# Optimization experiments

Measured on AMD Instinct MI355X. Metric: run time of the kernel, lower is better.

The kernel has to match this reference:

```python
import jax, jax.numpy as jnp
import numpy as np

HEADS = 8
DIM = 64
L = 2
P = 4  # hard-coded p_num in the torch module


def conv2d(x, w, b=None, pad=0, groups=1):
    y = jax.lax.conv_general_dilated(x, w, (1, 1), [(pad, pad), (pad, pad)],
        dimension_numbers=('NCHW', 'OIHW', 'NCHW'), feature_group_count=groups)
    return y if b is None else y + b[None, :, None, None]


def conv3d(x, w, pad=1, groups=1):
    return jax.lax.conv_general_dilated(x, w, (1, 1, 1), [(pad, pad)] * 3,
        dimension_numbers=('NCDHW', 'OIDHW', 'NCDHW'), feature_group_count=groups)


def pw(x, w):  # 1x1 conv, w: [O, C]
    return jnp.einsum('oc,bchw->bohw', w, x)


def layernorm(x, w, b):  # WithBias_LayerNorm over channel dim of NCHW
    mu = x.mean(axis=1, keepdims=True)
    var = ((x - mu) ** 2).mean(axis=1, keepdims=True)
    return (x - mu) / jnp.sqrt(var + 1e-5) * w[None, :, None, None] + b[None, :, None, None]


def l2n(x):  # F.normalize(dim=-1, p=2)
    return x / jnp.maximum(jnp.linalg.norm(x, axis=-1, keepdims=True), 1e-12)


def gelu(x):
    return jax.nn.gelu(x, approximate=False)


def spec_attn(x, mask, wq, wk, wv, dwq, dwk, dwv, resc, wp, mp1, mp2):
    b, c, h, w = x.shape
    ch = c // HEADS
    q = conv2d(pw(x, wq), dwq, pad=1, groups=c).reshape(b, HEADS, ch, h * w)
    k = conv2d(pw(x, wk), dwk, pad=1, groups=c).reshape(b, HEADS, ch, h * w)
    v = conv2d(pw(x, wv), dwv, pad=1, groups=c).reshape(b, HEADS, ch, h * w)
    q, k = l2n(q), l2n(k)
    att = jnp.einsum('bhcn,bhdn->bhcd', q, k) * resc[None, :, None, None]
    mb = pw(jax.nn.relu(conv2d(mask, mp1, pad=1)), mp2).mean(axis=(2, 3)).reshape(b, HEADS, ch)
    att = att + mb[:, :, None, :] - mb[:, :, :, None]
    att = jax.nn.softmax(att, axis=-1)
    out = jnp.einsum('bhcd,bhdn->bhcn', att, v).reshape(b, c, h, w)
    return pw(out, wp)


def ffn2d(x, w1, w2):  # PreNorm: dwconv3x3 (groups=dim, out=4*dim) -> GELU -> 1x1
    return pw(gelu(conv2d(x, w1, pad=1, groups=DIM)), w2)


def pol_attn(x, mask, wq, wk, wv, pwt, pb, resc, m1w, m1b, m2w, m2b):
    bp, c, h, w = x.shape
    bn = bp // P
    ch = c // HEADS
    xt = x.reshape(bn, P, c, h, w).transpose(0, 3, 4, 1, 2).reshape(bn * h * w, P, c)
    def heads_(t):
        return t.reshape(-1, P, HEADS, ch).transpose(0, 2, 1, 3)
    q = l2n(heads_(xt @ wq.T))
    k = l2n(heads_(xt @ wk.T))
    v = heads_(xt @ wv.T)
    att = jnp.einsum('bhpc,bhqc->bhpq', q, k) * resc[None, :, None, None]
    mg = pw(gelu(conv2d(mask, m1w, m1b, pad=1, groups=c)), m2w) + m2b[None, :, None, None]
    mg = mg.reshape(bn, P, c, h, w).mean(axis=2).transpose(0, 2, 3, 1).reshape(bn * h * w, P)
    att = att + (mg[:, None, :] - mg[:, :, None])[:, None]
    att = jax.nn.softmax(att, axis=-1)
    o = jnp.einsum('bhpq,bhqc->bhpc', att, v).transpose(0, 2, 1, 3).reshape(-1, P, c)
    o = o @ pwt.T + pb
    return o.reshape(bn, h, w, P, c).transpose(0, 3, 4, 1, 2).reshape(bp, c, h, w)


def ffn3d(x, w1, w2):  # PreNorm_Pols: 3D dwconv over (p,h,w) -> GELU -> 1x1x1
    bp, c, h, w = x.shape
    bn = bp // P
    y = x.reshape(bn, P, c, h, w).transpose(0, 2, 1, 3, 4)  # [bn, c, p, h, w]
    y = gelu(conv3d(y, w1, pad=1, groups=DIM))
    y = jnp.einsum('oc,bcdhw->bodhw', w2, y)
    return y.transpose(0, 2, 1, 3, 4).reshape(bp, c, h, w)


def forward(x, mask, sl1w, sl1b, sl2w, sl2b, swq, swk, swv, sdq, sdk, sdv, sresc, sproj,
            smp1, smp2, sf1, sf2, pl1w, pl1b, pl2w, pl2b, pwq, pwk, pwv, ppw, ppb, presc,
            pm1w, pm1b, pm2w, pm2b, pf1, pf2, fw1, fb1, fw2, fb2):
    # PSAM with type='pols': spectral branch + cross-polar branch + sigmoid fusion
    xs = x
    for i in range(L):
        xs = spec_attn(layernorm(xs, sl1w[i], sl1b[i]), mask, swq[i], swk[i], swv[i],
                       sdq[i], sdk[i], sdv[i], sresc[i], sproj[i], smp1[i], smp2[i]) + xs
        xs = ffn2d(layernorm(xs, sl2w[i], sl2b[i]), sf1[i], sf2[i]) + xs
    xp = x
    for i in range(L):
        xp = pol_attn(layernorm(xp, pl1w[i], pl1b[i]), mask, pwq[i], pwk[i], pwv[i],
                      ppw[i], ppb[i], presc[i], pm1w[i], pm1b[i], pm2w[i], pm2b[i]) + xp
        xp = ffn3d(layernorm(xp, pl2w[i], pl2b[i]), pf1[i], pf2[i]) + xp
    fu = jnp.concatenate([xs, xp], axis=1)
    a = jax.nn.sigmoid(conv2d(jax.nn.relu(pw(fu, fw1) + fb1[None, :, None, None]), fw2, fb2, pad=1))
    return a * xs + (1 - a) * xp


def setup_inputs():
    key = jax.random.key(0)
    D, H, Lb, B = DIM, HEADS, L, 8
    cnt = [0]
    def nrm(shape, s=0.02):
        cnt[0] += 1
        return jax.random.normal(jax.random.fold_in(key, cnt[0]), shape, jnp.float32) * s
    d = {}
    d['x'] = jax.random.normal(jax.random.fold_in(key, 1000), (B, D, 128, 128), jnp.float32)
    d['mask'] = jax.random.uniform(jax.random.fold_in(key, 1001), (B, D, 128, 128), jnp.float32)
    d['sl1w'] = jnp.ones((Lb, D)); d['sl1b'] = jnp.zeros((Lb, D))
    d['sl2w'] = jnp.ones((Lb, D)); d['sl2b'] = jnp.zeros((Lb, D))
    for n in ['swq', 'swk', 'swv', 'sproj', 'smp2']:
        d[n] = nrm((Lb, D, D))
    for n in ['sdq', 'sdk', 'sdv']:
        d[n] = nrm((Lb, D, 1, 3, 3))
    d['smp1'] = nrm((Lb, D, D, 3, 3))
    d['sresc'] = jnp.ones((Lb, H))
    d['sf1'] = nrm((Lb, 4 * D, 1, 3, 3)); d['sf2'] = nrm((Lb, D, 4 * D))
    d['pl1w'] = jnp.ones((Lb, D)); d['pl1b'] = jnp.zeros((Lb, D))
    d['pl2w'] = jnp.ones((Lb, D)); d['pl2b'] = jnp.zeros((Lb, D))
    for n in ['pwq', 'pwk', 'pwv', 'ppw', 'pm2w']:
        d[n] = nrm((Lb, D, D))
    d['ppb'] = jnp.zeros((Lb, D)); d['presc'] = jnp.ones((Lb, H))
    d['pm1w'] = nrm((Lb, D, 1, 3, 3)); d['pm1b'] = jnp.zeros((Lb, D)); d['pm2b'] = jnp.zeros((Lb, D))
    d['pf1'] = nrm((Lb, 4 * D, 1, 3, 3, 3)); d['pf2'] = nrm((Lb, D, 4 * D))
    d['fw1'] = nrm((D, 2 * D)); d['fb1'] = jnp.zeros((D,))
    d['fw2'] = nrm((D, D, 3, 3)); d['fb2'] = jnp.zeros((D,))
    return d


def reference(x, mask, sl1w, sl1b, sl2w, sl2b, swq, swk, swv, sdq, sdk, sdv, sresc, sproj,
              smp1, smp2, sf1, sf2, pl1w, pl1b, pl2w, pl2b, pwq, pwk, pwv, ppw, ppb, presc,
              pm1w, pm1b, pm2w, pm2b, pf1, pf2, fw1, fb1, fw2, fb2):
    return forward(x, mask, sl1w, sl1b, sl2w, sl2b, swq, swk, swv, sdq, sdk, sdv, sresc, sproj,
                   smp1, smp2, sf1, sf2, pl1w, pl1b, pl2w, pl2b, pwq, pwk, pwv, ppw, ppb, presc,
                   pm1w, pm1b, pm2w, pm2b, pf1, pf2, fw1, fb1, fw2, fb2)
```

## Files before the change

kernel.cpp:

```cpp
#include <hip/hip_runtime.h>
#include <math.h>

#define NPIX 16384
#define SBUF 8388608

__device__ __forceinline__ float gelu_f(float x){
    return 0.5f*x*(1.0f+erff(x*0.70710678118654752440f));
}
__device__ __forceinline__ float waveReduceSum(float v){
    #pragma unroll
    for(int off=32;off>0;off>>=1) v += __shfl_down(v, off);
    return v;
}

__global__ __launch_bounds__(256) void ln_kernel(const float* __restrict__ x,
        const float* __restrict__ w, const float* __restrict__ b, float* __restrict__ out){
    int idx = blockIdx.x*256 + threadIdx.x;
    int bb = idx >> 14, n = idx & 16383;
    const float* ip = x + ((size_t)bb<<20) + n;
    float v[64]; float s = 0.f;
    #pragma unroll
    for(int c=0;c<64;c++){ v[c] = ip[(size_t)c<<14]; s += v[c]; }
    float mu = s*(1.f/64.f); float ss = 0.f;
    #pragma unroll
    for(int c=0;c<64;c++){ float d = v[c]-mu; ss += d*d; }
    float r = rsqrtf(ss*(1.f/64.f) + 1e-5f);
    float* op = out + ((size_t)bb<<20) + n;
    #pragma unroll
    for(int c=0;c<64;c++) op[(size_t)c<<14] = (v[c]-mu)*r*w[c] + b[c];
}

__global__ __launch_bounds__(256) void pw_kernel(const float* __restrict__ in,
        const float* __restrict__ w, const float* __restrict__ bias,
        const float* __restrict__ res, float* __restrict__ out, int wPerB){
    __shared__ float wl[4096];
    int t = threadIdx.x;
    int idx = blockIdx.x*256 + t;
    int b = idx >> 14, n = idx & 16383;
    const float* wp = w + (wPerB ? b*4096 : 0);
    for(int i=t;i<4096;i+=256) wl[(i&63)*64 + (i>>6)] = wp[i];
    __syncthreads();
    float acc[64];
    if(bias){
        #pragma unroll
        for(int o=0;o<64;o++) acc[o] = bias[o];
    } else {
        #pragma unroll
        for(int o=0;o<64;o++) acc[o] = 0.f;
    }
    const float* ip = in + ((size_t)b<<20) + n;
    for(int c=0;c<64;c++){
        float v = ip[(size_t)c<<14];
        const float4* wv = (const float4*)&wl[c*64];
        #pragma unroll
        for(int o4=0;o4<16;o4++){
            float4 w4 = wv[o4];
            acc[o4*4+0] += w4.x*v; acc[o4*4+1] += w4.y*v;
            acc[o4*4+2] += w4.z*v; acc[o4*4+3] += w4.w*v;
        }
    }
    size_t baseo = ((size_t)b<<20) + n;
    if(res){
        #pragma unroll
        for(int o=0;o<64;o++) out[baseo+((size_t)o<<14)] = acc[o] + res[baseo+((size_t)o<<14)];
    } else {
        #pragma unroll
        for(int o=0;o<64;o++) out[baseo+((size_t)o<<14)] = acc[o];
    }
}

__global__ __launch_bounds__(256) void dw3x3_kernel(const float* __restrict__ in,
        const float* __restrict__ wd, float* __restrict__ out){
    int idx = blockIdx.x*256 + threadIdx.x;
    int n = idx & 16383; int bc = idx >> 14; int c = bc & 63;
    int y = n >> 7, x = n & 127;
    bool ym=y>0, yp=y<127, xm=x>0, xpv=x<127;
    const float* cp = in + ((size_t)bc<<14) + n;
    const float* wp = wd + c*9;
    float s = cp[0]*wp[4];
    if(ym){ s += cp[-128]*wp[1]; if(xm) s += cp[-129]*wp[0]; if(xpv) s += cp[-127]*wp[2]; }
    if(xm)  s += cp[-1]*wp[3];
    if(xpv) s += cp[1]*wp[5];
    if(yp){ s += cp[128]*wp[7]; if(xm) s += cp[127]*wp[6]; if(xpv) s += cp[129]*wp[8]; }
    out[idx] = s;
}

__global__ __launch_bounds__(256) void l2n_kernel(float* __restrict__ q){
    int bc = blockIdx.x;
    float* p = q + ((size_t)bc<<14);
    int t = threadIdx.x;
    float ss = 0.f;
    for(int n=t;n<NPIX;n+=256){ float v=p[n]; ss += v*v; }
    ss = waveReduceSum(ss);
    __shared__ float red[4];
    __shared__ float scale_s;
    if((t&63)==0) red[t>>6] = ss;
    __syncthreads();
    if(t==0) scale_s = 1.f/fmaxf(sqrtf(red[0]+red[1]+red[2]+red[3]), 1e-12f);
    __syncthreads();
    float sc = scale_s;
    for(int n=t;n<NPIX;n+=256) p[n] *= sc;
}

__global__ __launch_bounds__(256) void qk_kernel(const float* __restrict__ Q,
        const float* __restrict__ K, float* __restrict__ att){
    int blk = blockIdx.x;
    int c = blk & 7, bh = blk >> 3;
    const float* qp = Q + (((size_t)bh*8 + c)<<14);
    const float* kp = K + (((size_t)bh*8)<<14);
    float p[8] = {0,0,0,0,0,0,0,0};
    for(int n=threadIdx.x;n<NPIX;n+=256){
        float qv = qp[n];
        #pragma unroll
        for(int d=0;d<8;d++) p[d] += qv*kp[((size_t)d<<14)+n];
    }
    #pragma unroll
    for(int off=32;off>0;off>>=1){
        #pragma unroll
        for(int d=0;d<8;d++) p[d] += __shfl_down(p[d], off);
    }
    __shared__ float red[4][8];
    int wave = threadIdx.x>>6, lane = threadIdx.x&63;
    if(lane==0){
        #pragma unroll
        for(int d=0;d<8;d++) red[wave][d] = p[d];
    }
    __syncthreads();
    if(threadIdx.x<8){
        float s = red[0][threadIdx.x]+red[1][threadIdx.x]+red[2][threadIdx.x]+red[3][threadIdx.x];
        att[blk*8+threadIdx.x] = s;
    }
}

__global__ void zero512(float* __restrict__ p){
    p[blockIdx.x*256 + threadIdx.x] = 0.f;
}

__global__ __launch_bounds__(256) void mbconv4_kernel(const float* __restrict__ mask,
        const float* __restrict__ w, float* __restrict__ svec){
    __shared__ float wl[9216];
    __shared__ float red[4][16];
    int t = threadIdx.x;
    int og = blockIdx.x & 3;
    int pb = (blockIdx.x >> 2) & 31;
    int b  = blockIdx.x >> 7;
    const float* wp = w + (size_t)og*16*576;
    for(int i=t;i<9216;i+=256){
        int mo = i & 15, ck = i >> 4;
        wl[i] = wp[mo*576 + ck];
    }
    __syncthreads();
    int n0 = pb*512 + t;
    int n1 = n0 + 256;
    int y0 = n0>>7, x0 = n0&127;
    int y1 = n1>>7, x1 = n1&127;
    bool ym0=y0>0, yp0=y0<127, xm0=x0>0, xp0=x0<127;
    bool ym1=y1>0, yp1=y1<127, xm1=x1>0, xp1=x1<127;
    const float* mp = mask + ((size_t)b<<20);
    float acc0[16], acc1[16];
    #pragma unroll
    for(int o=0;o<16;o++){ acc0[o]=0.f; acc1[o]=0.f; }
    for(int c=0;c<64;c++){
        const float* cp0 = mp + ((size_t)c<<14) + n0;
        const float* cp1 = mp + ((size_t)c<<14) + n1;
        float ta[9], tb[9];
        ta[0] = (ym0&&xm0)? cp0[-129]:0.f;
        ta[1] =  ym0?       cp0[-128]:0.f;
        ta[2] = (ym0&&xp0)? cp0[-127]:0.f;
        ta[3] =  xm0?       cp0[-1]:0.f;
        ta[4] =             cp0[0];
        ta[5] =  xp0?       cp0[1]:0.f;
        ta[6] = (yp0&&xm0)? cp0[127]:0.f;
        ta[7] =  yp0?       cp0[128]:0.f;
        ta[8] = (yp0&&xp0)? cp0[129]:0.f;
        tb[0] = (ym1&&xm1)? cp1[-129]:0.f;
        tb[1] =  ym1?       cp1[-128]:0.f;
        tb[2] = (ym1&&xp1)? cp1[-127]:0.f;
        tb[3] =  xm1?       cp1[-1]:0.f;
        tb[4] =             cp1[0];
        tb[5] =  xp1?       cp1[1]:0.f;
        tb[6] = (yp1&&xm1)? cp1[127]:0.f;
        tb[7] =  yp1?       cp1[128]:0.f;
        tb[8] = (yp1&&xp1)? cp1[129]:0.f;
        #pragma unroll
        for(int k=0;k<9;k++){
            float va = ta[k], vb = tb[k];
            const float4* wv = (const float4*)&wl[(c*9+k)*16];
            #pragma unroll
            for(int o4=0;o4<4;o4++){
                float4 w4 = wv[o4];
                acc0[o4*4+0] += w4.x*va; acc0[o4*4+1] += w4.y*va;
                acc0[o4*4+2] += w4.z*va; acc0[o4*4+3] += w4.w*va;
                acc1[o4*4+0] += w4.x*vb; acc1[o4*4+1] += w4.y*vb;
                acc1[o4*4+2] += w4.z*vb; acc1[o4*4+3] += w4.w*vb;
            }
        }
    }
    int wave = t>>6, lane = t&63;
    #pragma unroll
    for(int m=0;m<16;m++){
        float v = waveReduceSum(fmaxf(acc0[m],0.f) + fmaxf(acc1[m],0.f));
        if(lane==0) red[wave][m] = v;
    }
    __syncthreads();
    if(t<16){
        float s = red[0][t]+red[1][t]+red[2][t]+red[3][t];
        atomicAdd(&svec[b*64 + og*16 + t], s);
    }
}

__global__ void spec_softmax_kernel(float* __restrict__ att, const float* __restrict__ svec,
        const float* __restrict__ smp2, const float* __restrict__ resc){
    int b = blockIdx.x, t = threadIdx.x;
    __shared__ float mb[64];
    float a = 0.f;
    for(int m=0;m<64;m++) a += smp2[t*64+m]*svec[b*64+m];
    mb[t] = a*(1.f/16384.f);
    __syncthreads();
    int h = t>>3, c = t&7;
    float* ap = att + (size_t)(b*8+h)*64 + c*8;
    float rs = resc[h];
    float v[8]; float mx = -1e30f;
    #pragma unroll
    for(int d=0;d<8;d++){ v[d] = ap[d]*rs + mb[h*8+d] - mb[h*8+c]; mx = fmaxf(mx, v[d]); }
    float s = 0.f;
    #pragma unroll
    for(int d=0;d<8;d++){ v[d] = expf(v[d]-mx); s += v[d]; }
    float inv = 1.f/s;
    #pragma unroll
    for(int d=0;d<8;d++) ap[d] = v[d]*inv;
}

__global__ void mmat_kernel(const float* __restrict__ att, const float* __restrict__ sproj,
        float* __restrict__ M){
    int b = blockIdx.x;
    for(int e=threadIdx.x;e<4096;e+=256){
        int o = e>>6, j = e&63;
        int h = j>>3, jj = j&7;
        float s = 0.f;
        #pragma unroll
        for(int cc=0;cc<8;cc++) s += sproj[o*64 + h*8+cc]*att[(size_t)(b*8+h)*64 + cc*8 + jj];
        M[b*4096 + e] = s;
    }
}

__global__ __launch_bounds__(256) void ffn2d_v3_kernel(const float* __restrict__ A,
        const float* __restrict__ w1, const float* __restrict__ w2, float* __restrict__ xs){
    __shared__ float w2l[4096];
    int t = threadIdx.x;
    int og = blockIdx.x & 3;
    int pb = (blockIdx.x >> 2) & 63;
    int b  = blockIdx.x >> 8;
    for(int i=t;i<4096;i+=256){
        int oo = i & 15, m = i >> 4;
        w2l[i] = w2[(og*16+oo)*256 + m];
    }
    __syncthreads();
    int n = pb*256 + t;
    int y = n>>7, x = n&127;
    bool ym=y>0, yp=y<127, xm=x>0, xpv=x<127;
    const float* ap = A + ((size_t)b<<20) + n;
    float acc[16];
    #pragma unroll
    for(int o=0;o<16;o++) acc[o] = 0.f;
    for(int c=0;c<64;c++){
        const float* cp = ap + ((size_t)c<<14);
        float t00 = (ym&&xm)? cp[-129]:0.f;
        float t01 =  ym?      cp[-128]:0.f;
        float t02 = (ym&&xpv)?cp[-127]:0.f;
        float t10 =  xm?      cp[-1]:0.f;
        float t11 =           cp[0];
        float t12 =  xpv?     cp[1]:0.f;
        float t20 = (yp&&xm)? cp[127]:0.f;
        float t21 =  yp?      cp[128]:0.f;
        float t22 = (yp&&xpv)?cp[129]:0.f;
        const float* w1c = w1 + c*36;
        #pragma unroll
        for(int j=0;j<4;j++){
            const float* wj = w1c + j*9;
            float cv = t00*wj[0]+t01*wj[1]+t02*wj[2]+t10*wj[3]+t11*wj[4]
                      +t12*wj[5]+t20*wj[6]+t21*wj[7]+t22*wj[8];
            float g = gelu_f(cv);
            const float4* wv = (const float4*)&w2l[(c*4+j)*16];
            #pragma unroll
            for(int o4=0;o4<4;o4++){
                float4 w4 = wv[o4];
                acc[o4*4+0] += w4.x*g; acc[o4*4+1] += w4.y*g;
                acc[o4*4+2] += w4.z*g; acc[o4*4+3] += w4.w*g;
            }
        }
    }
    size_t baseo = ((size_t)b<<20) + ((size_t)(og*16)<<14) + n;
    #pragma unroll
    for(int o=0;o<16;o++) xs[baseo+((size_t)o<<14)] += acc[o];
}

__global__ void wbar_kernel(const float* __restrict__ pm2w, const float* __restrict__ pm2b,
        float* __restrict__ wbar){
    int t = threadIdx.x;
    float s = 0.f;
    for(int o=0;o<64;o++) s += pm2w[o*64+t];
    wbar[t] = s*(1.f/64.f);
    if(t==0){
        float sb = 0.f;
        for(int o=0;o<64;o++) sb += pm2b[o];
        wbar[64] = sb*(1.f/64.f);
    }
}

__global__ __launch_bounds__(256) void mg_kernel(const float* __restrict__ mask,
        const float* __restrict__ w1, const float* __restrict__ b1,
        const float* __restrict__ wbar, float* __restrict__ mg){
    int idx = blockIdx.x*256 + threadIdx.x;
    int b = idx>>14, n = idx&16383;
    int y = n>>7, x = n&127;
    bool ym=y>0, yp=y<127, xm=x>0, xpv=x<127;
    const float* ap = mask + ((size_t)b<<20) + n;
    float acc = wbar[64];
    for(int c=0;c<64;c++){
        const float* cp = ap + ((size_t)c<<14);
        const float* wj = w1 + c*9;
        float cv = b1[c] + cp[0]*wj[4];
        if(ym){ cv += cp[-128]*wj[1]; if(xm) cv += cp[-129]*wj[0]; if(xpv) cv += cp[-127]*wj[2]; }
        if(xm)  cv += cp[-1]*wj[3];
        if(xpv) cv += cp[1]*wj[5];
        if(yp){ cv += cp[128]*wj[7]; if(xm) cv += cp[127]*wj[6]; if(xpv) cv += cp[129]*wj[8]; }
        acc += wbar[c]*gelu_f(cv);
    }
    mg[idx] = acc;
}

__global__ __launch_bounds__(256) void att_pol_kernel(const float* __restrict__ Q,
        const float* __restrict__ K, const float* __restrict__ V,
        const float* __restrict__ mg, const float* __restrict__ resc, float* __restrict__ O){
    int idx = blockIdx.x*256 + threadIdx.x;
    int bn = idx>>14, n = idx&16383;
    float mgv[4];
    #pragma unroll
    for(int p=0;p<4;p++) mgv[p] = mg[(((bn<<2)+p)<<14) + n];
    for(int h=0;h<8;h++){
        size_t base = ((size_t)bn<<22) + ((size_t)h<<17) + n;
        float q[4][8], k[4][8], v[4][8];
        #pragma unroll
        for(int p=0;p<4;p++){
            size_t pb = base + ((size_t)p<<20);
            #pragma unroll
            for(int j=0;j<8;j++){
                size_t o = pb + ((size_t)j<<14);
                q[p][j] = Q[o]; k[p][j] = K[o]; v[p][j] = V[o];
            }
        }
        #pragma unroll
        for(int p=0;p<4;p++){
            float sq=0.f, sk=0.f;
            #pragma unroll
            for(int j=0;j<8;j++){ sq += q[p][j]*q[p][j]; sk += k[p][j]*k[p][j]; }
            float iq = 1.f/fmaxf(sqrtf(sq),1e-12f), ik = 1.f/fmaxf(sqrtf(sk),1e-12f);
            #pragma unroll
            for(int j=0;j<8;j++){ q[p][j]*=iq; k[p][j]*=ik; }
        }
        float rs = resc[h];
        float att[4][4];
        #pragma unroll
        for(int p=0;p<4;p++){
            #pragma unroll
            for(int r=0;r<4;r++){
                float d = 0.f;
                #pragma unroll
                for(int j=0;j<8;j++) d += q[p][j]*k[r][j];
                att[p][r] = rs*d + mgv[r] - mgv[p];
            }
        }
        #pragma unroll
        for(int p=0;p<4;p++){
            float mx = fmaxf(fmaxf(att[p][0],att[p][1]),fmaxf(att[p][2],att[p][3]));
            float s = 0.f;
            #pragma unroll
            for(int r=0;r<4;r++){ att[p][r] = expf(att[p][r]-mx); s += att[p][r]; }
            float inv = 1.f/s;
            #pragma unroll
            for(int r=0;r<4;r++) att[p][r] *= inv;
        }
        #pragma unroll
        for(int p=0;p<4;p++){
            size_t pb = base + ((size_t)p<<20);
            #pragma unroll
            for(int j=0;j<8;j++){
                float o = att[p][0]*v[0][j]+att[p][1]*v[1][j]+att[p][2]*v[2][j]+att[p][3]*v[3][j];
                O[pb + ((size_t)j<<14)] = o;
            }
        }
    }
}

__global__ __launch_bounds__(256) void ffn3d_v3_kernel(const float* __restrict__ A,
        const float* __restrict__ w1, const float* __restrict__ w2, float* __restrict__ xp){
    __shared__ float w2l[4096];
    int t = threadIdx.x;
    int og = blockIdx.x & 3;
    int pbk = (blockIdx.x >> 2) & 63;
    int bp = blockIdx.x >> 8;
    for(int i=t;i<4096;i+=256){
        int oo = i & 15, m = i >> 4;
        w2l[i] = w2[(og*16+oo)*256 + m];
    }
    __syncthreads();
    int bn = bp>>2, p = bp&3;
    int n = pbk*256 + t;
    int y = n>>7, x = n&127;
    bool ym=y>0, yp=y<127, xm=x>0, xpv=x<127;
    float acc[16];
    #pragma unroll
    for(int o=0;o<16;o++) acc[o] = 0.f;
    for(int c=0;c<64;c++){
        float tap[27];
        #pragma unroll
        for(int dz=0;dz<3;dz++){
            int pp = p + dz - 1;
            if(pp < 0 || pp > 3){
                #pragma unroll
                for(int k9=0;k9<9;k9++) tap[dz*9+k9] = 0.f;
            } else {
                const float* cp = A + ((size_t)((bn<<2)+pp)<<20) + ((size_t)c<<14) + n;
                tap[dz*9+0] = (ym&&xm)? cp[-129]:0.f;
                tap[dz*9+1] =  ym?      cp[-128]:0.f;
                tap[dz*9+2] = (ym&&xpv)?cp[-127]:0.f;
                tap[dz*9+3] =  xm?      cp[-1]:0.f;
                tap[dz*9+4] =           cp[0];
                tap[dz*9+5] =  xpv?     cp[1]:0.f;
                tap[dz*9+6] = (yp&&xm)? cp[127]:0.f;
                tap[dz*9+7] =  yp?      cp[128]:0.f;
                tap[dz*9+8] = (yp&&xpv)?cp[129]:0.f;
            }
        }
        const float* w1c = w1 + c*108;
        #pragma unroll
        for(int j=0;j<4;j++){
            const float* wj = w1c + j*27;
            float cv = 0.f;
            #pragma unroll
            for(int k27=0;k27<27;k27++) cv += tap[k27]*wj[k27];
            float g = gelu_f(cv);
            const float4* wv = (const float4*)&w2l[(c*4+j)*16];
            #pragma unroll
            for(int o4=0;o4<4;o4++){
                float4 w4 = wv[o4];
                acc[o4*4+0] += w4.x*g; acc[o4*4+1] += w4.y*g;
                acc[o4*4+2] += w4.z*g; acc[o4*4+3] += w4.w*g;
            }
        }
    }
    size_t baseo = ((size_t)bp<<20) + ((size_t)(og*16)<<14) + n;
    #pragma unroll
    for(int o=0;o<16;o++) xp[baseo+((size_t)o<<14)] += acc[o];
}

__global__ __launch_bounds__(256) void fuse1_kernel(const float* __restrict__ xs,
        const float* __restrict__ xp, const float* __restrict__ fw1,
        const float* __restrict__ fb1, float* __restrict__ T){
    __shared__ float wl[8192];
    int t = threadIdx.x;
    for(int i=t;i<8192;i+=256) wl[(i&127)*64 + (i>>7)] = fw1[i];
    __syncthreads();
    int idx = blockIdx.x*256 + t;
    int b = idx>>14, n = idx&16383;
    float acc[64];
    #pragma unroll
    for(int o=0;o<64;o++) acc[o] = fb1[o];
    const float* ip = xs + ((size_t)b<<20) + n;
    for(int c=0;c<64;c++){
        float v = ip[(size_t)c<<14];
        const float4* wv = (const float4*)&wl[c*64];
        #pragma unroll
        for(int o4=0;o4<16;o4++){
            float4 w4 = wv[o4];
            acc[o4*4+0] += w4.x*v; acc[o4*4+1] += w4.y*v;
            acc[o4*4+2] += w4.z*v; acc[o4*4+3] += w4.w*v;
        }
    }
    const float* ip2 = xp + ((size_t)b<<20) + n;
    for(int c=0;c<64;c++){
        float v = ip2[(size_t)c<<14];
        const float4* wv = (const float4*)&wl[(64+c)*64];
        #pragma unroll
        for(int o4=0;o4<16;o4++){
            float4 w4 = wv[o4];
            acc[o4*4+0] += w4.x*v; acc[o4*4+1] += w4.y*v;
            acc[o4*4+2] += w4.z*v; acc[o4*4+3] += w4.w*v;
        }
    }
    size_t baseo = ((size_t)b<<20) + n;
    #pragma unroll
    for(int o=0;o<64;o++) T[baseo+((size_t)o<<14)] = fmaxf(acc[o], 0.f);
}

__global__ __launch_bounds__(256) void fuse2v2_kernel(const float* __restrict__ T,
        const float* __restrict__ fw2, const float* __restrict__ fb2,
        const float* __restrict__ xs, const float* __restrict__ xp, float* __restrict__ out){
    __shared__ float wl[9216];
    int t = threadIdx.x;
    int og = blockIdx.x & 3;
    int pb = (blockIdx.x >> 2) & 31;
    int b  = blockIdx.x >> 7;
    const float* wp = fw2 + (size_t)og*16*576;
    for(int i=t;i<9216;i+=256){
        int mo = i & 15, ck = i >> 4;
        wl[i] = wp[mo*576 + ck];
    }
    __syncthreads();
    int n0 = pb*512 + t;
    int n1 = n0 + 256;
    int y0 = n0>>7, x0 = n0&127;
    int y1 = n1>>7, x1 = n1&127;
    bool ym0=y0>0, yp0=y0<127, xm0=x0>0, xp0=x0<127;
    bool ym1=y1>0, yp1=y1<127, xm1=x1>0, xp1=x1<127;
    const float* tp = T + ((size_t)b<<20);
    float acc0[16], acc1[16];
    #pragma unroll
    for(int o=0;o<16;o++){ acc0[o]=0.f; acc1[o]=0.f; }
    for(int c=0;c<64;c++){
        const float* cp0 = tp + ((size_t)c<<14) + n0;
        const float* cp1 = tp + ((size_t)c<<14) + n1;
        float ta[9], tb[9];
        ta[0] = (ym0&&xm0)? cp0[-129]:0.f;
        ta[1] =  ym0?       cp0[-128]:0.f;
        ta[2] = (ym0&&xp0)? cp0[-127]:0.f;
        ta[3] =  xm0?       cp0[-1]:0.f;
        ta[4] =             cp0[0];
        ta[5] =  xp0?       cp0[1]:0.f;
        ta[6] = (yp0&&xm0)? cp0[127]:0.f;
        ta[7] =  yp0?       cp0[128]:0.f;
        ta[8] = (yp0&&xp0)? cp0[129]:0.f;
        tb[0] = (ym1&&xm1)? cp1[-129]:0.f;
        tb[1] =  ym1?       cp1[-128]:0.f;
        tb[2] = (ym1&&xp1)? cp1[-127]:0.f;
        tb[3] =  xm1?       cp1[-1]:0.f;
        tb[4] =             cp1[0];
        tb[5] =  xp1?       cp1[1]:0.f;
        tb[6] = (yp1&&xm1)? cp1[127]:0.f;
        tb[7] =  yp1?       cp1[128]:0.f;
        tb[8] = (yp1&&xp1)? cp1[129]:0.f;
        #pragma unroll
        for(int k=0;k<9;k++){
            float va = ta[k], vb = tb[k];
            const float4* wv = (const float4*)&wl[(c*9+k)*16];
            #pragma unroll
            for(int o4=0;o4<4;o4++){
                float4 w4 = wv[o4];
                acc0[o4*4+0] += w4.x*va; acc0[o4*4+1] += w4.y*va;
                acc0[o4*4+2] += w4.z*va; acc0[o4*4+3] += w4.w*va;
                acc1[o4*4+0] += w4.x*vb; acc1[o4*4+1] += w4.y*vb;
                acc1[o4*4+2] += w4.z*vb; acc1[o4*4+3] += w4.w*vb;
            }
        }
    }
    #pragma unroll
    for(int m=0;m<16;m++){
        int o = og*16 + m;
        float bias = fb2[o];
        size_t i0 = ((size_t)b<<20) + ((size_t)o<<14) + n0;
        size_t i1 = ((size_t)b<<20) + ((size_t)o<<14) + n1;
        float a0 = 1.f/(1.f+expf(-(acc0[m]+bias)));
        float a1 = 1.f/(1.f+expf(-(acc1[m]+bias)));
        out[i0] = a0*xs[i0] + (1.f-a0)*xp[i0];
        out[i1] = a1*xs[i1] + (1.f-a1)*xp[i1];
    }
}

extern "C" void kernel_launch(void* const* d_in, const int* in_sizes, int n_in,
                              void* d_out, int out_size, void* d_ws, size_t ws_size,
                              hipStream_t stream) {
    const float* x     = (const float*)d_in[0];
    const float* mask  = (const float*)d_in[1];
    const float* sl1w  = (const float*)d_in[2];
    const float* sl1b  = (const float*)d_in[3];
    const float* sl2w  = (const float*)d_in[4];
    const float* sl2b  = (const float*)d_in[5];
    const float* swq   = (const float*)d_in[6];
    const float* swk   = (const float*)d_in[7];
    const float* swv   = (const float*)d_in[8];
    const float* sproj = (const float*)d_in[9];
    const float* smp2  = (const float*)d_in[10];
    const float* sdq   = (const float*)d_in[11];
    const float* sdk   = (const float*)d_in[12];
    const float* sdv   = (const float*)d_in[13];
    const float* smp1  = (const float*)d_in[14];
    const float* sresc = (const float*)d_in[15];
    const float* sf1   = (const float*)d_in[16];
    const float* sf2   = (const float*)d_in[17];
    const float* pl1w  = (const float*)d_in[18];
    const float* pl1b  = (const float*)d_in[19];
    const float* pl2w  = (const float*)d_in[20];
    const float* pl2b  = (const float*)d_in[21];
    const float* pwq   = (const float*)d_in[22];
    const float* pwk   = (const float*)d_in[23];
    const float* pwv   = (const float*)d_in[24];
    const float* ppw   = (const float*)d_in[25];
    const float* pm2w  = (const float*)d_in[26];
    const float* ppb   = (const float*)d_in[27];
    const float* presc = (const float*)d_in[28];
    const float* pm1w  = (const float*)d_in[29];
    const float* pm1b  = (const float*)d_in[30];
    const float* pm2b  = (const float*)d_in[31];
    const float* pf1   = (const float*)d_in[32];
    const float* pf2   = (const float*)d_in[33];
    const float* fw1   = (const float*)d_in[34];
    const float* fb1   = (const float*)d_in[35];
    const float* fw2   = (const float*)d_in[36];
    const float* fb2   = (const float*)d_in[37];

    float* ws_f = (float*)d_ws;
    float* xs = ws_f;
    float* xp = ws_f + (size_t)SBUF;
    float* A  = ws_f + 2*(size_t)SBUF;
    float* Q  = ws_f + 3*(size_t)SBUF;
    float* K  = ws_f + 4*(size_t)SBUF;
    float* V  = ws_f + 5*(size_t)SBUF;
    float* small = ws_f + 6*(size_t)SBUF;
    float* mg   = small;
    float* att  = mg + 131072;
    float* svec = att + 4096;
    float* M    = svec + 512;
    float* wbar = M + 32768;
    float* stage = (float*)d_out;
    float* Tf = Q;

    hipMemcpyAsync(xs, x, (size_t)SBUF*4, hipMemcpyDeviceToDevice, stream);
    hipMemcpyAsync(xp, x, (size_t)SBUF*4, hipMemcpyDeviceToDevice, stream);

    for(int i=0;i<2;i++){
        ln_kernel<<<512,256,0,stream>>>(xs, sl1w+i*64, sl1b+i*64, A);
        pw_kernel<<<512,256,0,stream>>>(A, swq+i*4096, nullptr, nullptr, stage, 0);
        dw3x3_kernel<<<32768,256,0,stream>>>(stage, sdq+i*576, Q);
        pw_kernel<<<512,256,0,stream>>>(A, swk+i*4096, nullptr, nullptr, stage, 0);
        dw3x3_kernel<<<32768,256,0,stream>>>(stage, sdk+i*576, K);
        pw_kernel<<<512,256,0,stream>>>(A, swv+i*4096, nullptr, nullptr, stage, 0);
        dw3x3_kernel<<<32768,256,0,stream>>>(stage, sdv+i*576, V);
        l2n_kernel<<<512,256,0,stream>>>(Q);
        l2n_kernel<<<512,256,0,stream>>>(K);
        qk_kernel<<<512,256,0,stream>>>(Q, K, att);
        zero512<<<2,256,0,stream>>>(svec);
        mbconv4_kernel<<<1024,256,0,stream>>>(mask, smp1+i*36864, svec);
        spec_softmax_kernel<<<8,64,0,stream>>>(att, svec, smp2+i*4096, sresc+i*8);
        mmat_kernel<<<8,256,0,stream>>>(att, sproj+i*4096, M);
        pw_kernel<<<512,256,0,stream>>>(V, M, nullptr, xs, xs, 1);
        ln_kernel<<<512,256,0,stream>>>(xs, sl2w+i*64, sl2b+i*64, A);
        ffn2d_v3_kernel<<<2048,256,0,stream>>>(A, sf1+i*2304, sf2+i*16384, xs);
    }
    for(int i=0;i<2;i++){
        ln_kernel<<<512,256,0,stream>>>(xp, pl1w+i*64, pl1b+i*64, A);
        pw_kernel<<<512,256,0,stream>>>(A, pwq+i*4096, nullptr, nullptr, Q, 0);
        pw_kernel<<<512,256,0,stream>>>(A, pwk+i*4096, nullptr, nullptr, K, 0);
        pw_kernel<<<512,256,0,stream>>>(A, pwv+i*4096, nullptr, nullptr, V, 0);
        wbar_kernel<<<1,64,0,stream>>>(pm2w+i*4096, pm2b+i*64, wbar);
        mg_kernel<<<512,256,0,stream>>>(mask, pm1w+i*576, pm1b+i*64, wbar, mg);
        att_pol_kernel<<<128,256,0,stream>>>(Q, K, V, mg, presc+i*8, stage);
        pw_kernel<<<512,256,0,stream>>>(stage, ppw+i*4096, ppb+i*64, xp, xp, 0);
        ln_kernel<<<512,256,0,stream>>>(xp, pl2w+i*64, pl2b+i*64, A);
        ffn3d_v3_kernel<<<2048,256,0,stream>>>(A, pf1+i*6912, pf2+i*16384, xp);
    }
    fuse1_kernel<<<512,256,0,stream>>>(xs, xp, fw1, fb1, Tf);
    fuse2v2_kernel<<<1024,256,0,stream>>>(Tf, fw2, fb2, xs, xp, (float*)d_out);
}
```

Before: 2.933 ms.

## Fold L2 normalization into QK reduction and split polarization attention by head

The spectral branch no longer rewrites Q and K with separate L2-normalization passes. Instead, qk2_kernel accumulates the squared norms alongside the Q·K dot products, and the softmax kernel applies the inverse norms as scalars. The QK reduction is also split into four spatial chunks that combine through atomicAdd after a zeroing launch, which gives 2048 blocks instead of 512. The polarization attention kernel now parallelizes over heads as well, launching 1024 blocks instead of 128. This removes two full read/write passes over Q and K and raises occupancy, at the cost of atomics and floating-point results that now depend on summation order.

Result: faster. 2.800 ms (-4.6%).

```diff
diff --git a/kernel.cpp b/kernel.cpp
--- a/kernel.cpp
+++ b/kernel.cpp
@@ -85,32 +85,23 @@
     out[idx] = s;
 }
 
-__global__ __launch_bounds__(256) void l2n_kernel(float* __restrict__ q){
-    int bc = blockIdx.x;
-    float* p = q + ((size_t)bc<<14);
-    int t = threadIdx.x;
-    float ss = 0.f;
-    for(int n=t;n<NPIX;n+=256){ float v=p[n]; ss += v*v; }
-    ss = waveReduceSum(ss);
-    __shared__ float red[4];
-    __shared__ float scale_s;
-    if((t&63)==0) red[t>>6] = ss;
-    __syncthreads();
-    if(t==0) scale_s = 1.f/fmaxf(sqrtf(red[0]+red[1]+red[2]+red[3]), 1e-12f);
-    __syncthreads();
-    float sc = scale_s;
-    for(int n=t;n<NPIX;n+=256) p[n] *= sc;
-}
-
-__global__ __launch_bounds__(256) void qk_kernel(const float* __restrict__ Q,
-        const float* __restrict__ K, float* __restrict__ att){
+__global__ void zero5632(float* __restrict__ p){
+    p[blockIdx.x*256 + threadIdx.x] = 0.f;
+}
+
+__global__ __launch_bounds__(256) void qk2_kernel(const float* __restrict__ Q,
+        const float* __restrict__ K, float* __restrict__ att,
+        float* __restrict__ qn, float* __restrict__ kn){
     int blk = blockIdx.x;
-    int c = blk & 7, bh = blk >> 3;
+    int c = blk & 7, bh = (blk>>3) & 63, chunk = blk >> 9;
     const float* qp = Q + (((size_t)bh*8 + c)<<14);
     const float* kp = K + (((size_t)bh*8)<<14);
     float p[8] = {0,0,0,0,0,0,0,0};
-    for(int n=threadIdx.x;n<NPIX;n+=256){
-        float qv = qp[n];
+    float qsq = 0.f, ksq = 0.f;
+    int n0 = chunk*4096;
+    for(int n = n0 + threadIdx.x; n < n0+4096; n += 256){
+        float qv = qp[n]; qsq += qv*qv;
+        float kc = kp[((size_t)c<<14)+n]; ksq += kc*kc;
         #pragma unroll
         for(int d=0;d<8;d++) p[d] += qv*kp[((size_t)d<<14)+n];
     }
@@ -118,22 +109,23 @@
     for(int off=32;off>0;off>>=1){
         #pragma unroll
         for(int d=0;d<8;d++) p[d] += __shfl_down(p[d], off);
-    }
-    __shared__ float red[4][8];
+        qsq += __shfl_down(qsq, off);
+        ksq += __shfl_down(ksq, off);
+    }
+    __shared__ float red[4][10];
     int wave = threadIdx.x>>6, lane = threadIdx.x&63;
     if(lane==0){
         #pragma unroll
         for(int d=0;d<8;d++) red[wave][d] = p[d];
-    }
-    __syncthreads();
-    if(threadIdx.x<8){
+        red[wave][8] = qsq; red[wave][9] = ksq;
+    }
+    __syncthreads();
+    if(threadIdx.x<10){
         float s = red[0][threadIdx.x]+red[1][threadIdx.x]+red[2][threadIdx.x]+red[3][threadIdx.x];
-        att[blk*8+threadIdx.x] = s;
-    }
-}
-
-__global__ void zero512(float* __restrict__ p){
-    p[blockIdx.x*256 + threadIdx.x] = 0.f;
+        if(threadIdx.x<8)       atomicAdd(&att[(size_t)(bh*8+c)*8 + threadIdx.x], s);
+        else if(threadIdx.x==8) atomicAdd(&qn[bh*8+c], s);
+        else                    atomicAdd(&kn[bh*8+c], s);
+    }
 }
 
 __global__ __launch_bounds__(256) void mbconv4_kernel(const float* __restrict__ mask,
@@ -209,8 +201,9 @@
     }
 }
 
-__global__ void spec_softmax_kernel(float* __restrict__ att, const float* __restrict__ svec,
-        const float* __restrict__ smp2, const float* __restrict__ resc){
+__global__ void spec_softmax2_kernel(float* __restrict__ att, const float* __restrict__ svec,
+        const float* __restrict__ smp2, const float* __restrict__ resc,
+        const float* __restrict__ qn, const float* __restrict__ kn){
     int b = blockIdx.x, t = threadIdx.x;
     __shared__ float mb[64];
     float a = 0.f;
@@ -220,9 +213,13 @@
     int h = t>>3, c = t&7;
     float* ap = att + (size_t)(b*8+h)*64 + c*8;
     float rs = resc[h];
+    float iqc = 1.f/fmaxf(sqrtf(qn[(b*8+h)*8+c]), 1e-12f);
+    float ik[8];
+    #pragma unroll
+    for(int d=0;d<8;d++) ik[d] = 1.f/fmaxf(sqrtf(kn[(b*8+h)*8+d]), 1e-12f);
     float v[8]; float mx = -1e30f;
     #pragma unroll
-    for(int d=0;d<8;d++){ v[d] = ap[d]*rs + mb[h*8+d] - mb[h*8+c]; mx = fmaxf(mx, v[d]); }
+    for(int d=0;d<8;d++){ v[d] = ap[d]*rs*iqc*ik[d] + mb[h*8+d] - mb[h*8+c]; mx = fmaxf(mx, v[d]); }
     float s = 0.f;
     #pragma unroll
     for(int d=0;d<8;d++){ v[d] = expf(v[d]-mx); s += v[d]; }
@@ -330,65 +327,64 @@
     mg[idx] = acc;
 }
 
-__global__ __launch_bounds__(256) void att_pol_kernel(const float* __restrict__ Q,
+__global__ __launch_bounds__(256) void att_pol2_kernel(const float* __restrict__ Q,
         const float* __restrict__ K, const float* __restrict__ V,
         const float* __restrict__ mg, const float* __restrict__ resc, float* __restrict__ O){
-    int idx = blockIdx.x*256 + threadIdx.x;
+    int h = blockIdx.x & 7;
+    int idx = (blockIdx.x>>3)*256 + threadIdx.x;
     int bn = idx>>14, n = idx&16383;
     float mgv[4];
     #pragma unroll
     for(int p=0;p<4;p++) mgv[p] = mg[(((bn<<2)+p)<<14) + n];
-    for(int h=0;h<8;h++){
-        size_t base = ((size_t)bn<<22) + ((size_t)h<<17) + n;
-        float q[4][8], k[4][8], v[4][8];
-        #pragma unroll
-        for(int p=0;p<4;p++){
-            size_t pb = base + ((size_t)p<<20);
+    size_t base = ((size_t)bn<<22) + ((size_t)h<<17) + n;
+    float q[4][8], k[4][8], v[4][8];
+    #pragma unroll
+    for(int p=0;p<4;p++){
+        size_t pb = base + ((size_t)p<<20);
+        #pragma unroll
+        for(int j=0;j<8;j++){
+            size_t o = pb + ((size_t)j<<14);
+            q[p][j] = Q[o]; k[p][j] = K[o]; v[p][j] = V[o];
+        }
+    }
+    #pragma unroll
+    for(int p=0;p<4;p++){
+        float sq=0.f, sk=0.f;
+        #pragma unroll
+        for(int j=0;j<8;j++){ sq += q[p][j]*q[p][j]; sk += k[p][j]*k[p][j]; }
+        float iq = 1.f/fmaxf(sqrtf(sq),1e-12f), ik = 1.f/fmaxf(sqrtf(sk),1e-12f);
+        #pragma unroll
+        for(int j=0;j<8;j++){ q[p][j]*=iq; k[p][j]*=ik; }
+    }
+    float rs = resc[h];
+    float att[4][4];
+    #pragma unroll
+    for(int p=0;p<4;p++){
+        #pragma unroll
+        for(int r=0;r<4;r++){
+            float d = 0.f;
             #pragma unroll
-            for(int j=0;j<8;j++){
-                size_t o = pb + ((size_t)j<<14);
-                q[p][j] = Q[o]; k[p][j] = K[o]; v[p][j] = V[o];
-            }
-        }
-        #pragma unroll
-        for(int p=0;p<4;p++){
-            float sq=0.f, sk=0.f;
-            #pragma unroll
-            for(int j=0;j<8;j++){ sq += q[p][j]*q[p][j]; sk += k[p][j]*k[p][j]; }
-            float iq = 1.f/fmaxf(sqrtf(sq),1e-12f), ik = 1.f/fmaxf(sqrtf(sk),1e-12f);
-            #pragma unroll
-            for(int j=0;j<8;j++){ q[p][j]*=iq; k[p][j]*=ik; }
-        }
-        float rs = resc[h];
-        float att[4][4];
-        #pragma unroll
-        for(int p=0;p<4;p++){
-            #pragma unroll
-            for(int r=0;r<4;r++){
-                float d = 0.f;
-                #pragma unroll
-                for(int j=0;j<8;j++) d += q[p][j]*k[r][j];
-                att[p][r] = rs*d + mgv[r] - mgv[p];
-            }
-        }
-        #pragma unroll
-        for(int p=0;p<4;p++){
-            float mx = fmaxf(fmaxf(att[p][0],att[p][1]),fmaxf(att[p][2],att[p][3]));
-            float s = 0.f;
-            #pragma unroll
-            for(int r=0;r<4;r++){ att[p][r] = expf(att[p][r]-mx); s += att[p][r]; }
-            float inv = 1.f/s;
-            #pragma unroll
-            for(int r=0;r<4;r++) att[p][r] *= inv;
-        }
-        #pragma unroll
-        for(int p=0;p<4;p++){
-            size_t pb = base + ((size_t)p<<20);
-            #pragma unroll
-            for(int j=0;j<8;j++){
-                float o = att[p][0]*v[0][j]+att[p][1]*v[1][j]+att[p][2]*v[2][j]+att[p][3]*v[3][j];
-                O[pb + ((size_t)j<<14)] = o;
-            }
+            for(int j=0;j<8;j++) d += q[p][j]*k[r][j];
+            att[p][r] = rs*d + mgv[r] - mgv[p];
+        }
+    }
+    #pragma unroll
+    for(int p=0;p<4;p++){
+        float mx = fmaxf(fmaxf(att[p][0],att[p][1]),fmaxf(att[p][2],att[p][3]));
+        float s = 0.f;
+        #pragma unroll
+        for(int r=0;r<4;r++){ att[p][r] = expf(att[p][r]-mx); s += att[p][r]; }
+        float inv = 1.f/s;
+        #pragma unroll
+        for(int r=0;r<4;r++) att[p][r] *= inv;
+    }
+    #pragma unroll
+    for(int p=0;p<4;p++){
+        size_t pb = base + ((size_t)p<<20);
+        #pragma unroll
+        for(int j=0;j<8;j++){
+            float o = att[p][0]*v[0][j]+att[p][1]*v[1][j]+att[p][2]*v[2][j]+att[p][3]*v[3][j];
+            O[pb + ((size_t)j<<14)] = o;
         }
     }
 }
@@ -620,7 +616,9 @@
     float* mg   = small;
     float* att  = mg + 131072;
     float* svec = att + 4096;
-    float* M    = svec + 512;
+    float* qn   = svec + 512;
+    float* kn   = qn + 512;
+    float* M    = kn + 512;
     float* wbar = M + 32768;
     float* stage = (float*)d_out;
     float* Tf = Q;
@@ -636,12 +634,10 @@
         dw3x3_kernel<<<32768,256,0,stream>>>(stage, sdk+i*576, K);
         pw_kernel<<<512,256,0,stream>>>(A, swv+i*4096, nullptr, nullptr, stage, 0);
         dw3x3_kernel<<<32768,256,0,stream>>>(stage, sdv+i*576, V);
-        l2n_kernel<<<512,256,0,stream>>>(Q);
-        l2n_kernel<<<512,256,0,stream>>>(K);
-        qk_kernel<<<512,256,0,stream>>>(Q, K, att);
-        zero512<<<2,256,0,stream>>>(svec);
+        zero5632<<<22,256,0,stream>>>(att);
+        qk2_kernel<<<2048,256,0,stream>>>(Q, K, att, qn, kn);
         mbconv4_kernel<<<1024,256,0,stream>>>(mask, smp1+i*36864, svec);
-        spec_softmax_kernel<<<8,64,0,stream>>>(att, svec, smp2+i*4096, sresc+i*8);
+        spec_softmax2_kernel<<<8,64,0,stream>>>(att, svec, smp2+i*4096, sresc+i*8, qn, kn);
         mmat_kernel<<<8,256,0,stream>>>(att, sproj+i*4096, M);
         pw_kernel<<<512,256,0,stream>>>(V, M, nullptr, xs, xs, 1);
         ln_kernel<<<512,256,0,stream>>>(xs, sl2w+i*64, sl2b+i*64, A);
@@ -654,7 +650,7 @@
         pw_kernel<<<512,256,0,stream>>>(A, pwv+i*4096, nullptr, nullptr, V, 0);
         wbar_kernel<<<1,64,0,stream>>>(pm2w+i*4096, pm2b+i*64, wbar);
         mg_kernel<<<512,256,0,stream>>>(mask, pm1w+i*576, pm1b+i*64, wbar, mg);
-        att_pol_kernel<<<128,256,0,stream>>>(Q, K, V, mg, presc+i*8, stage);
+        att_pol2_kernel<<<1024,256,0,stream>>>(Q, K, V, mg, presc+i*8, stage);
         pw_kernel<<<512,256,0,stream>>>(stage, ppw+i*4096, ppb+i*64, xp, xp, 0);
         ln_kernel<<<512,256,0,stream>>>(xp, pl2w+i*64, pl2b+i*64, A);
         ffn3d_v3_kernel<<<2048,256,0,stream>>>(A, pf1+i*6912, pf2+i*16384, xp);
```
